# Kernel tuning notes

Measured on AMD Instinct MI355X. Metric: run time of the kernel, lower is better.

Reference implementation:

```python
import jax, jax.numpy as jnp
import numpy as np

NSIDE = 64
NLAT = 4 * NSIDE - 1        # 255 iso-latitude rings
NLON = 4 * NSIDE            # 256 = max pixels per ring
NPIX = 12 * NSIDE * NSIDE   # 49152 HEALPix pixels
LMAX = NLAT                 # 255
MMAX = NLON // 2 + 1        # 129
BATCH, CHAN = 8, 32


def _ring_geometry():
    # HEALPix ring scheme: ring r (0-based), 1-based i=r+1
    #  north cap i<nside: nph=4i, phi shift 0.5
    #  equatorial nside<=i<=3*nside: nph=4*nside, shift alternates {0,0.5}
    #  south cap: mirror of north cap
    nph = np.zeros(NLAT, np.int64)
    shift = np.zeros(NLAT, np.float64)
    for r in range(NLAT):
        i = r + 1
        if i < NSIDE:
            nph[r], shift[r] = 4 * i, 0.5
        elif i <= 3 * NSIDE:
            nph[r], shift[r] = 4 * NSIDE, 0.5 * ((i - NSIDE + 1) % 2)
        else:
            nph[r], shift[r] = 4 * (NLAT - r), 0.5
    offs = np.concatenate([[0], np.cumsum(nph)[:-1]])
    p = np.arange(NLON)
    mask = (p[None, :] < nph[:, None])                       # [nlat, nlon]
    idx = (offs[:, None] + p[None, :]) * mask                # padded -> 0
    phase = 2.0 * np.pi * (p[None, :] + shift[:, None]) / nph[:, None] * mask
    return idx.astype(np.int32), mask.astype(np.float32), phase.astype(np.float32)


def setup_inputs() -> dict:
    key = jax.random.key(0)
    k1, k2, k3 = jax.random.split(key, 3)
    idx, mask, phase = _ring_geometry()
    x = jax.random.normal(k1, (BATCH, CHAN, NPIX), jnp.float32)
    pct = jax.random.normal(k2, (MMAX, LMAX, NLAT), jnp.float32) * 0.1  # Legendre table stand-in
    w = jax.random.uniform(k3, (NLAT,), jnp.float32)                    # per-ring quadrature weights
    return {"x": x, "pct": pct, "w": w,
            "ring_index": jnp.asarray(idx),
            "ring_mask": jnp.asarray(mask),
            "phase": jnp.asarray(phase)}


def _healpix_rfft_real(x, ring_index, ring_mask, phase):
    # x: [..., npix] -> per-ring DFT coefficients as real pairs [..., nlat, mmax, 2]
    rings = x[..., ring_index] * ring_mask                 # [..., nlat, nlon]
    m = jnp.arange(MMAX, dtype=phase.dtype)
    ang = phase[:, :, None] * m                            # [nlat, nlon, mmax]
    fr = jnp.einsum('...kp,kpm->...km', rings, jnp.cos(ang))
    fi = -jnp.einsum('...kp,kpm->...km', rings, jnp.sin(ang))
    return jnp.stack([fr, fi], axis=-1)                    # n=2 is view_as_real axis


def reference(x, pct, w, ring_index, ring_mask, phase):
    # healpix ring rFFT, then Legendre contraction (einsum '...kmn,mlk->...lmn')
    f = _healpix_rfft_real(x, ring_index, ring_mask, phase)  # [..., nlat, mmax, 2]
    weights = pct * w                                        # [mmax, lmax, nlat]
    out = jnp.einsum('...kmn,mlk->...lmn', f, weights)       # [..., lmax, mmax, 2]
    return out
```

## Files before the change

kernel.cpp:

```cpp
#include <hip/hip_runtime.h>

#define NLAT 255
#define NLON 256
#define NPIX 49152
#define MMAX 129
#define MCS  258
#define NTBL 65
#define TROWS 264

typedef unsigned short ushort_t;
typedef __attribute__((ext_vector_type(8)))  short  bf16x8;
typedef __attribute__((ext_vector_type(4)))  short  short4v;
typedef __attribute__((ext_vector_type(16))) float  f32x16;
typedef __attribute__((ext_vector_type(4)))  float  float4v;

__device__ __forceinline__ ushort_t f2bf(float f) {
    union { float f; unsigned u; } v; v.f = f;
    unsigned r = v.u + 0x7FFFu + ((v.u >> 16) & 1u);
    return (ushort_t)(r >> 16);
}
__device__ __forceinline__ float bf2f(ushort_t h) {
    union { unsigned u; float f; } v; v.u = ((unsigned)h) << 16;
    return v.f;
}

__global__ __launch_bounds__(256) void prepK(const float* __restrict__ pct,
                                             const float* __restrict__ w,
                                             ushort_t* __restrict__ pctwF) {
    const int m  = blockIdx.x;
    const int l0 = blockIdx.y * 32;
    const int t  = threadIdx.x;
    const float wk = (t < NLAT) ? w[t] : 0.f;
    const int kg = t >> 3, j = t & 7;
    for (int l = l0; l < l0 + 32; ++l) {
        float v = 0.f;
        if (l < NLAT && t < NLAT)
            v = pct[((size_t)m * NLAT + l) * NLAT + t] * wk;
        pctwF[(((size_t)m * 32 + kg) * 256 + l) * 8 + j] = f2bf(v);
    }
}

__global__ __launch_bounds__(256) void trigK(const float* __restrict__ phase,
                                             const float* __restrict__ mask,
                                             ushort_t* __restrict__ Ttab3) {
    const int tt  = blockIdx.x;
    const int mcs = blockIdx.y;
    const int p   = threadIdx.x;
    const int r   = (tt < 63) ? tt : (tt == 63 ? 63 : 64);
    float val = 0.f;
    if (mcs < MCS) {
        float ph = phase[r * NLON + p];
        float mk = mask[r * NLON + p];
        float fm = (float)(mcs >> 1);
        float s, c;
        __sincosf(ph * fm, &s, &c);
        val = (mcs & 1) ? (-s * mk) : (c * mk);
    }
    const int pcc = p >> 6, c = (p >> 3) & 7, j = p & 7;
    Ttab3[((((size_t)tt * 4 + pcc) * 8 + c) * TROWS + mcs) * 8 + j] = f2bf(val);
}

__global__ __launch_bounds__(256, 2) void stageA(const float* __restrict__ x,
                                                 const int* __restrict__ ring_index,
                                                 const ushort_t* __restrict__ Ttab3,
                                                 ushort_t* __restrict__ f1) {
    __shared__ __align__(16) ushort_t Rs[2][64 * 72];

    const int b0 = blockIdx.x * 64;
    const int r  = blockIdx.y;
    const int i1 = r + 1;
    const int nph = (i1 < 64) ? 4 * i1 : (i1 <= 192 ? 256 : 4 * (256 - i1));
    const int tbl = (i1 < 64) ? r : (i1 <= 192 ? (63 + (((i1 - 63) & 1) ^ 1)) : 254 - r);
    const int base = ring_index[r * NLON];
    const int nchunks = (nph + 63) >> 6;

    const int t    = threadIdx.x;
    const int lane = t & 63;
    const int wid  = t >> 6;
    const int wrow = wid >> 1, wcol = wid & 1;
    const int lg   = lane >> 5;
    const int lc   = lane & 31;

    f32x16 acc[5];
#pragma unroll
    for (int tau = 0; tau < 5; ++tau)
#pragma unroll
        for (int q = 0; q < 16; ++q) acc[tau][q] = 0.f;

    int trow[5];
#pragma unroll
    for (int tau = 0; tau < 5; ++tau) {
        int rr = tau * 64 + wcol * 32 + lc;
        trow[tau] = rr > (TROWS - 1) ? (TROWS - 1) : rr;
    }

    float4v rx[4];
    const int p0 = (t & 15) * 4;
    auto ldX = [&](int pc) {
        const bool ok = (pc + p0) < nph;
#pragma unroll
        for (int pass = 0; pass < 4; ++pass) {
            int bc = (t >> 4) + pass * 16;
            float4v v = {0.f, 0.f, 0.f, 0.f};
            if (ok) v = *(const float4v*)(x + (size_t)(b0 + bc) * NPIX + base + pc + p0);
            rx[pass] = v;
        }
    };
    auto stX = [&](ushort_t* dst) {
#pragma unroll
        for (int pass = 0; pass < 4; ++pass) {
            int bc = (t >> 4) + pass * 16;
            short4v h;
            h[0] = (short)f2bf(rx[pass][0]); h[1] = (short)f2bf(rx[pass][1]);
            h[2] = (short)f2bf(rx[pass][2]); h[3] = (short)f2bf(rx[pass][3]);
            *(short4v*)(dst + bc * 72 + p0) = h;
        }
    };

    ldX(0);
    stX(Rs[0]);
    __syncthreads();

    for (int c = 0; c < nchunks; ++c) {
        const int pc = c << 6;
        const bool more = (c + 1) < nchunks;
        const ushort_t* slab = Ttab3 + (size_t)(tbl * 4 + c) * (8 * TROWS * 8);

        bf16x8 bfr[4][5];
#pragma unroll
        for (int ks = 0; ks < 4; ++ks) {
            const ushort_t* bcol = slab + (size_t)(ks * 2 + lg) * (TROWS * 8);
#pragma unroll
            for (int tau = 0; tau < 4; ++tau)
                bfr[ks][tau] = *(const bf16x8*)(bcol + trow[tau] * 8);
            if (wcol == 0)
                bfr[ks][4] = *(const bf16x8*)(bcol + trow[4] * 8);
        }
        if (more) ldX(pc + 64);

        const ushort_t* Rcur = Rs[c & 1];
#pragma unroll
        for (int ks = 0; ks < 4; ++ks) {
            bf16x8 a = *(const bf16x8*)(Rcur + (wrow * 32 + lc) * 72 + ks * 16 + lg * 8);
#pragma unroll
            for (int tau = 0; tau < 4; ++tau)
                acc[tau] = __builtin_amdgcn_mfma_f32_32x32x16_bf16(a, bfr[ks][tau], acc[tau], 0, 0, 0);
            if (wcol == 0)
                acc[4] = __builtin_amdgcn_mfma_f32_32x32x16_bf16(a, bfr[ks][4], acc[4], 0, 0, 0);
        }
        if (more) stX(Rs[(c + 1) & 1]);
        __syncthreads();
    }

    ushort_t* Olds = Rs[0];
#pragma unroll
    for (int tau = 0; tau < 5; ++tau) {
        __syncthreads();
        {
            const int mcsl = wcol * 32 + lc;
#pragma unroll
            for (int q = 0; q < 16; ++q) {
                int bcl = wrow * 32 + 4 * lg + (q & 3) + 8 * (q >> 2);
                Olds[mcsl * 72 + bcl] = f2bf(acc[tau][q]);
            }
        }
        __syncthreads();
        {
            int row = t >> 2;
            int mcs = tau * 64 + row;
            if (mcs < MCS) {
                int m = mcs >> 1, n = mcs & 1;
                size_t gbase = ((size_t)m * NLAT + r) * 512 + n * 256 + b0 + (t & 3) * 16;
#pragma unroll
                for (int j = 0; j < 2; ++j) {
                    bf16x8 v = *(const bf16x8*)(Olds + row * 72 + (t & 3) * 16 + j * 8);
                    *(bf16x8*)(f1 + gbase + j * 8) = v;
                }
            }
        }
    }
}

__global__ __launch_bounds__(256) void transK(const ushort_t* __restrict__ f1,
                                              ushort_t* __restrict__ f1tF) {
    __shared__ __align__(16) ushort_t T[64][72];
    const int m  = blockIdx.x;
    const int k0 = blockIdx.y * 64;
    const int b0 = blockIdx.z * 64;
    const int t  = threadIdx.x;
#pragma unroll
    for (int it = 0; it < 2; ++it) {
        int id = t + it * 256;
        int kk = id >> 3, ch = id & 7;
        int k  = k0 + kk;
        bf16x8 v = {0,0,0,0,0,0,0,0};
        if (k < NLAT)
            v = *(const bf16x8*)(f1 + ((size_t)m * NLAT + k) * 512 + b0 + ch * 8);
        *(bf16x8*)(&T[kk][ch * 8]) = v;
    }
    __syncthreads();
#pragma unroll
    for (int it = 0; it < 2; ++it) {
        int id  = t + it * 256;
        int bb  = id & 63, ch8 = id >> 6;
        bf16x8 v;
#pragma unroll
        for (int j = 0; j < 8; ++j) v[j] = T[ch8 * 8 + j][bb];
        *(bf16x8*)(f1tF + (((size_t)m * 32 + (k0 >> 3) + ch8) * 512 + b0 + bb) * 8) = v;
    }
}

__global__ __launch_bounds__(256, 3) void stageB(const ushort_t* __restrict__ f1tF,
                                                 const ushort_t* __restrict__ pctwF,
                                                 ushort_t* __restrict__ otmp) {
    __shared__ __align__(16) ushort_t SB[24576];
    ushort_t* Es = SB;

    const int id = blockIdx.x;
    const int m  = ((id >> 5) << 3) | (id & 7);
    if (m >= MMAX) return;
    const int b2t = ((id >> 3) & 3) * 128;

    const int t    = threadIdx.x;
    const int lane = t & 63;
    const int wid  = t >> 6;
    const int wrow = wid >> 1, wlcol = wid & 1;
    const int lg   = lane >> 5, lc = lane & 31;

    f32x16 acc[2][4];
#pragma unroll
    for (int i = 0; i < 2; ++i)
#pragma unroll
        for (int j = 0; j < 4; ++j)
#pragma unroll
            for (int q = 0; q < 16; ++q) acc[i][j][q] = 0.f;

    const ushort_t* aSrc = f1tF  + (size_t)m * 32 * 512 * 8;
    const ushort_t* wSrc = pctwF + (size_t)m * 32 * 256 * 8;

    auto STAGE = [&](int buf, int c) {
#pragma unroll
        for (int u = 0; u < 2; ++u) {
            int sA   = wid * 2 + u;
            int kg   = c * 4 + (sA >> 1);
            int half = sA & 1;
            const ushort_t* src = aSrc + ((size_t)kg * 512 + b2t + half * 64) * 8 + lane * 8;
            __builtin_amdgcn_global_load_lds(
                (const __attribute__((address_space(1))) void*)src,
                (__attribute__((address_space(3))) void*)(SB + buf * 4096 + sA * 512),
                16, 0, 0);
        }
#pragma unroll
        for (int u = 0; u < 4; ++u) {
            int sW = wid * 4 + u;
            int kg = c * 4 + (sW >> 2);
            int q  = sW & 3;
            const ushort_t* src = wSrc + ((size_t)kg * 256 + q * 64) * 8 + lane * 8;
            __builtin_amdgcn_global_load_lds(
                (const __attribute__((address_space(1))) void*)src,
                (__attribute__((address_space(3))) void*)(SB + 8192 + buf * 8192 + sW * 512),
                16, 0, 0);
        }
    };

    STAGE(0, 0);
    __syncthreads();
    int buf = 0;
    for (int c = 0; c < 8; ++c, buf ^= 1) {
        if (c + 1 < 8) STAGE(buf ^ 1, c + 1);
        const ushort_t* A = SB + buf * 4096;
        const ushort_t* W = SB + 8192 + buf * 8192;
#pragma unroll
        for (int ks = 0; ks < 2; ++ks) {
            const int kgl = ks * 2 + lg;
            bf16x8 a0 = *(const bf16x8*)(A + (kgl * 128 + wrow * 64 + lc) * 8);
            bf16x8 a1 = *(const bf16x8*)(A + (kgl * 128 + wrow * 64 + 32 + lc) * 8);
#pragma unroll
            for (int jj = 0; jj < 4; ++jj) {
                bf16x8 b = *(const bf16x8*)(W + (kgl * 256 + wlcol * 128 + jj * 32 + lc) * 8);
                acc[0][jj] = __builtin_amdgcn_mfma_f32_32x32x16_bf16(a0, b, acc[0][jj], 0, 0, 0);
                acc[1][jj] = __builtin_amdgcn_mfma_f32_32x32x16_bf16(a1, b, acc[1][jj], 0, 0, 0);
            }
        }
        __syncthreads();
    }

#pragma unroll
    for (int h = 0; h < 2; ++h) {
        if (h) __syncthreads();
        if (wlcol == h) {
#pragma unroll
            for (int i = 0; i < 2; ++i)
#pragma unroll
                for (int jj = 0; jj < 4; ++jj)
#pragma unroll
                    for (int q = 0; q < 16; ++q) {
                        int bl = wrow * 64 + i * 32 + 4 * lg + (q & 3) + 8 * (q >> 2);
                        Es[bl * 136 + jj * 32 + lc] = f2bf(acc[i][jj][q]);
                    }
        }
        __syncthreads();
#pragma unroll
        for (int it = 0; it < 8; ++it) {
            int id2 = t + it * 256;
            int row = id2 >> 4, ch = id2 & 15;
            bf16x8 v = *(const bf16x8*)(Es + row * 136 + ch * 8);
            *(bf16x8*)(otmp + (((size_t)m * 512 + b2t + row) << 8) + h * 128 + ch * 8) = v;
        }
    }
}

__global__ __launch_bounds__(256) void permuteK(const ushort_t* __restrict__ otmp,
                                                float* __restrict__ out) {
    __shared__ ushort_t L[MCS * 66];
    const int bc = blockIdx.x;
    const int l0 = blockIdx.y * 64;
    const int t  = threadIdx.x;
    const int ll = t & 63;
    const int l  = l0 + ll;
#pragma unroll 4
    for (int it = 0; it < 65; ++it) {
        int mn = (t >> 6) + it * 4;
        if (mn < MCS) {
            int mm = mn >> 1, n = mn & 1;
            ushort_t v = 0;
            if (l < NLAT)
                v = otmp[(((size_t)mm * 512 + n * 256 + bc) << 8) + l];
            L[mn * 66 + ll] = v;
        }
    }
    __syncthreads();
    for (int ll2 = 0; ll2 < 64; ++ll2) {
        int lo = l0 + ll2;
        if (lo >= NLAT) break;
        size_t rowb = ((size_t)bc * NLAT + lo) * MCS;
        out[rowb + t] = bf2f(L[t * 66 + ll2]);
        if (t < 2)
            out[rowb + 256 + t] = bf2f(L[(256 + t) * 66 + ll2]);
    }
}

extern "C" void kernel_launch(void* const* d_in, const int* in_sizes, int n_in,
                              void* d_out, int out_size, void* d_ws, size_t ws_size,
                              hipStream_t stream) {
    const float* x          = (const float*)d_in[0];
    const float* pct        = (const float*)d_in[1];
    const float* w          = (const float*)d_in[2];
    const int*   ring_index = (const int*)d_in[3];
    const float* ring_mask  = (const float*)d_in[4];
    const float* phase      = (const float*)d_in[5];
    float* out = (float*)d_out;

    char* wsb = (char*)d_ws;
    char* ob  = (char*)d_out;
    ushort_t* otmp  = (ushort_t*)wsb;
    ushort_t* f1    = (ushort_t*)(wsb + 33552384);
    ushort_t* f1tF  = (ushort_t*)ob;
    ushort_t* pctwF = (ushort_t*)(ob + 33816576);
    ushort_t* Ttab3 = (ushort_t*)(ob + 50724864);

    prepK   <<<dim3(MMAX, 8),     256, 0, stream>>>(pct, w, pctwF);
    trigK   <<<dim3(NTBL, TROWS), 256, 0, stream>>>(phase, ring_mask, Ttab3);
    stageA  <<<dim3(4, NLAT),     256, 0, stream>>>(x, ring_index, Ttab3, f1);
    transK  <<<dim3(MMAX, 4, 8),  256, 0, stream>>>(f1, f1tF);
    stageB  <<<dim3(544),         256, 0, stream>>>(f1tF, pctwF, otmp);
    permuteK<<<dim3(256, 4),      256, 0, stream>>>(otmp, out);
}
```

Baseline: 119.1 us.

## Merge weight-prep and trig-table kernels into one launch with vectorized stores

Fuses the Legendre-weight preparation and the trig-table generation into a single kernel, splitting the grid by block index so one launch is saved. The prep path now reads 16 contiguous pct values per thread with float4 loads, scales them by w, and writes two 16-byte bf16 vectors. The trig path writes 8 bf16 values at once instead of scalar 2-byte stores. The aim is to cut launch overhead and the poorly coalesced scalar stores, at the cost of unaligned vector loads of pct and a longer strided loop in each trig block.

```diff
diff --git a/kernel.cpp b/kernel.cpp
--- a/kernel.cpp
+++ b/kernel.cpp
@@ -7,12 +7,14 @@
 #define MCS  258
 #define NTBL 65
 #define TROWS 264
+#define NPREP (MMAX * 16)
 
 typedef unsigned short ushort_t;
 typedef __attribute__((ext_vector_type(8)))  short  bf16x8;
 typedef __attribute__((ext_vector_type(4)))  short  short4v;
 typedef __attribute__((ext_vector_type(16))) float  f32x16;
 typedef __attribute__((ext_vector_type(4)))  float  float4v;
+typedef __attribute__((ext_vector_type(4), aligned(4))) float float4u;
 
 __device__ __forceinline__ ushort_t f2bf(float f) {
     union { float f; unsigned u; } v; v.f = f;
@@ -24,40 +26,71 @@
     return v.f;
 }
 
-__global__ __launch_bounds__(256) void prepK(const float* __restrict__ pct,
-                                             const float* __restrict__ w,
-                                             ushort_t* __restrict__ pctwF) {
-    const int m  = blockIdx.x;
-    const int l0 = blockIdx.y * 32;
-    const int t  = threadIdx.x;
-    const float wk = (t < NLAT) ? w[t] : 0.f;
-    const int kg = t >> 3, j = t & 7;
-    for (int l = l0; l < l0 + 32; ++l) {
-        float v = 0.f;
-        if (l < NLAT && t < NLAT)
-            v = pct[((size_t)m * NLAT + l) * NLAT + t] * wk;
-        pctwF[(((size_t)m * 32 + kg) * 256 + l) * 8 + j] = f2bf(v);
-    }
-}
-
-__global__ __launch_bounds__(256) void trigK(const float* __restrict__ phase,
-                                             const float* __restrict__ mask,
-                                             ushort_t* __restrict__ Ttab3) {
-    const int tt  = blockIdx.x;
-    const int mcs = blockIdx.y;
-    const int p   = threadIdx.x;
-    const int r   = (tt < 63) ? tt : (tt == 63 ? 63 : 64);
-    float val = 0.f;
-    if (mcs < MCS) {
-        float ph = phase[r * NLON + p];
-        float mk = mask[r * NLON + p];
-        float fm = (float)(mcs >> 1);
-        float s, c;
-        __sincosf(ph * fm, &s, &c);
-        val = (mcs & 1) ? (-s * mk) : (c * mk);
-    }
-    const int pcc = p >> 6, c = (p >> 3) & 7, j = p & 7;
-    Ttab3[((((size_t)tt * 4 + pcc) * 8 + c) * TROWS + mcs) * 8 + j] = f2bf(val);
+__global__ __launch_bounds__(256) void prepTrigK(const float* __restrict__ pct,
+                                                 const float* __restrict__ w,
+                                                 const float* __restrict__ phase,
+                                                 const float* __restrict__ mask,
+                                                 ushort_t* __restrict__ pctwF,
+                                                 ushort_t* __restrict__ Ttab3) {
+    const int bid = blockIdx.x;
+    const int t   = threadIdx.x;
+    if (bid < NPREP) {
+        const int m   = bid >> 4;
+        const int kg0 = (bid & 15) * 2;
+        const int k0  = kg0 * 8;
+        const int l   = t;
+        float vals[16];
+        if (l < NLAT) {
+            const float* src = pct + ((size_t)m * NLAT + l) * NLAT + k0;
+            if (k0 + 16 <= NLAT) {
+#pragma unroll
+                for (int c = 0; c < 4; ++c) {
+                    float4u pv = *(const float4u*)(src + c * 4);
+                    float4v wv = *(const float4v*)(w + k0 + c * 4);
+#pragma unroll
+                    for (int j = 0; j < 4; ++j) vals[c * 4 + j] = pv[j] * wv[j];
+                }
+            } else {
+#pragma unroll
+                for (int j = 0; j < 16; ++j) {
+                    int k = k0 + j;
+                    vals[j] = (k < NLAT) ? src[j] * w[k] : 0.f;
+                }
+            }
+        } else {
+#pragma unroll
+            for (int j = 0; j < 16; ++j) vals[j] = 0.f;
+        }
+        bf16x8 h0, h1;
+#pragma unroll
+        for (int j = 0; j < 8; ++j) { h0[j] = (short)f2bf(vals[j]); h1[j] = (short)f2bf(vals[8 + j]); }
+        *(bf16x8*)(pctwF + (((size_t)m * 32 + kg0)     * 256 + l) * 8) = h0;
+        *(bf16x8*)(pctwF + (((size_t)m * 32 + kg0 + 1) * 256 + l) * 8) = h1;
+    } else {
+        const int idx = bid - NPREP;
+        const int tt  = idx >> 2;
+        const int pcc = idx & 3;
+        const int r   = (tt < 63) ? tt : (tt == 63 ? 63 : 64);
+        for (int i = t; i < 8 * TROWS; i += 256) {
+            const int c   = i / TROWS;
+            const int mcs = i - c * TROWS;
+            bf16x8 h = {0,0,0,0,0,0,0,0};
+            if (mcs < MCS) {
+                const float fm = (float)(mcs >> 1);
+#pragma unroll
+                for (int j = 0; j < 8; ++j) {
+                    int p = pcc * 64 + c * 8 + j;
+                    float ph = phase[r * NLON + p];
+                    float mk = mask[r * NLON + p];
+                    float s, cs;
+                    __sincosf(ph * fm, &s, &cs);
+                    float val = (mcs & 1) ? (-s * mk) : (cs * mk);
+                    h[j] = (short)f2bf(val);
+                }
+            }
+            *(bf16x8*)(Ttab3 + ((((size_t)tt * 4 + pcc) * 8 + c) * TROWS + mcs) * 8) = h;
+        }
+    }
 }
 
 __global__ __launch_bounds__(256, 2) void stageA(const float* __restrict__ x,
@@ -359,8 +392,8 @@
     ushort_t* pctwF = (ushort_t*)(ob + 33816576);
     ushort_t* Ttab3 = (ushort_t*)(ob + 50724864);
 
-    prepK   <<<dim3(MMAX, 8),     256, 0, stream>>>(pct, w, pctwF);
-    trigK   <<<dim3(NTBL, TROWS), 256, 0, stream>>>(phase, ring_mask, Ttab3);
+    prepTrigK<<<dim3(NPREP + NTBL * 4), 256, 0, stream>>>(pct, w, phase, ring_mask,
+                                                          pctwF, Ttab3);
     stageA  <<<dim3(4, NLAT),     256, 0, stream>>>(x, ring_index, Ttab3, f1);
     transK  <<<dim3(MMAX, 4, 8),  256, 0, stream>>>(f1, f1tF);
     stageB  <<<dim3(544),         256, 0, stream>>>(f1tF, pctwF, otmp);
```

New measurement: 118.6 us. No clear change (-0.5%).
